# Kernel tuning notes

Hardware: AMD Instinct MI355X
Metric: run time of the kernel (lower is better)

## Reference

```python
import jax, jax.numpy as jnp
import numpy as np

B, S, D, H = 4, 2048, 1024, 16
DH = D // H  # 64
NEG = -1e9


def setup_inputs() -> dict:
    key = jax.random.key(0)
    k1, k2, k3 = jax.random.split(key, 3)
    x = jax.random.normal(k1, (B, S, D), dtype=jnp.float32)
    w_attn = jax.random.normal(k2, (D, 3 * D), dtype=jnp.float32) * 0.02
    b_attn = jnp.zeros((3 * D,), dtype=jnp.float32)
    w_proj = jax.random.normal(k3, (D, D), dtype=jnp.float32) * 0.02
    b_proj = jnp.zeros((D,), dtype=jnp.float32)
    return {"x": x, "w_attn": w_attn, "b_attn": b_attn, "w_proj": w_proj, "b_proj": b_proj}


def reference(x, w_attn, b_attn, w_proj, b_proj):
    # c_attn: fused QKV projection (Conv1D with rf=1 == dense layer)
    qkv = x @ w_attn + b_attn  # [B,S,3D]
    q, k, v = jnp.split(qkv, 3, axis=-1)

    def split_heads(t):  # [B,S,D] -> [B,H,S,DH]
        return t.reshape(B, S, H, DH).transpose(0, 2, 1, 3)

    q, k, v = split_heads(q), split_heads(k), split_heads(v)

    # scaled scores with additive causal mask (as w*b + -1e9*(1-b))
    w = jnp.einsum("bhqd,bhkd->bhqk", q, k) / jnp.sqrt(jnp.float32(DH))
    causal = jnp.tril(jnp.ones((S, S), dtype=w.dtype))[None, None]
    w = w * causal + NEG * (1.0 - causal)
    w = jax.nn.softmax(w, axis=-1)
    # attn_dropout / resid_dropout: p=0 (eval) -> identity

    a = jnp.einsum("bhqk,bhkd->bhqd", w, v)  # [B,H,S,DH]
    a = a.transpose(0, 2, 1, 3).reshape(B, S, D)  # merge heads
    return a @ w_proj + b_proj
```

## Files before the change

### kernel.cpp

```cpp
#include <hip/hip_runtime.h>


typedef short  s8v   __attribute__((ext_vector_type(8)));
typedef float  f32x4 __attribute__((ext_vector_type(4)));
typedef float  f32x16 __attribute__((ext_vector_type(16)));
typedef unsigned short u16;
typedef u16    u16x4 __attribute__((ext_vector_type(4)));
typedef unsigned int u32;
typedef u32    u32x2 __attribute__((ext_vector_type(2)));

__device__ __forceinline__ u16 f2b(float f) {
  union { float f; unsigned u; } v; v.f = f;
  unsigned r = v.u + 0x7FFFu + ((v.u >> 16) & 1u);
  return (u16)(r >> 16);
}
__device__ __forceinline__ u32 cvtpk(float lo, float hi) {
  u32 r; asm("v_cvt_pk_bf16_f32 %0, %1, %2" : "=v"(r) : "v"(lo), "v"(hi)); return r;
}
__device__ __forceinline__ void plswap(u32 &d, u32 &s) {
  asm volatile("v_permlane32_swap_b32 %0, %1" : "+v"(d), "+v"(s));
}
__device__ __forceinline__ void gll16(const void* g, void* l) {
  __builtin_amdgcn_global_load_lds((const __attribute__((address_space(1))) void*)g,
                                   (__attribute__((address_space(3))) void*)l, 16, 0, 0);
}

#define QSCALE 0.18033688011112042f

__global__ __launch_bounds__(256) void k_cvt(const float* __restrict__ in,
                                             u16* __restrict__ out, int n4) {
  int t = blockIdx.x * 256 + threadIdx.x;
  if (t < n4) {
    f32x4 f = ((const f32x4*)in)[t];
    u16x4 o;
    o[0] = f2b(f[0]); o[1] = f2b(f[1]); o[2] = f2b(f[2]); o[3] = f2b(f[3]);
    ((u16x4*)out)[t] = o;
  }
}

__global__ __launch_bounds__(256) void k_tr(const float* __restrict__ in,
                                            u16* __restrict__ out, int R, int C) {
  __shared__ float tile[32][33];
  int c0 = blockIdx.x * 32, r0 = blockIdx.y * 32;
  int tx = threadIdx.x, ty = threadIdx.y;
#pragma unroll
  for (int j = 0; j < 4; j++)
    tile[ty + j * 8][tx] = in[(size_t)(r0 + ty + j * 8) * C + c0 + tx];
  __syncthreads();
#pragma unroll
  for (int j = 0; j < 4; j++)
    out[(size_t)(c0 + ty + j * 8) * R + r0 + tx] = f2b(tile[tx][ty + j * 8]);
}

__device__ __forceinline__ void gemm_tile(const u16* bA, const u16* bB,
                                          f32x4 (&acc)[4][8],
                                          int wr, int wc, int lr, int lg) {
  s8v af[4], bfr[8];
#pragma unroll
  for (int m = 0; m < 4; m++) {
    const int row = wr + m * 16 + lr;
    af[m] = *(const s8v*)&bA[row * 32 + (lg ^ ((row >> 1) & 3)) * 8];
  }
#pragma unroll
  for (int n = 0; n < 8; n++) {
    const int row = wc + n * 16 + lr;
    bfr[n] = *(const s8v*)&bB[row * 32 + (lg ^ ((row >> 1) & 3)) * 8];
  }
  __builtin_amdgcn_s_setprio(1);
#pragma unroll
  for (int m = 0; m < 4; m++)
#pragma unroll
    for (int n = 0; n < 8; n++)
      acc[m][n] = __builtin_amdgcn_mfma_f32_16x16x32_bf16(af[m], bfr[n], acc[m][n], 0, 0, 0);
  __builtin_amdgcn_s_setprio(0);
}

template <int EPI>
__global__ __launch_bounds__(256, 2) void k_gemm(
    const u16* __restrict__ A, const u16* __restrict__ Bt,
    const float* __restrict__ bias,
    u16* __restrict__ qb, u16* __restrict__ kb, u16* __restrict__ vb,
    float* __restrict__ outf, int M, int N, int K) {
  __shared__ u16 lA[3][4096];
  __shared__ u16 lB[3][8192];
  const int tid = threadIdx.x;
  const int lane = tid & 63, w = tid >> 6;
  const int wr = (w >> 1) * 64, wc = (w & 1) * 128;
  const int lr = lane & 15, lg = lane >> 4;

  const int nwg = gridDim.x * gridDim.y;
  const int bid = blockIdx.y * gridDim.x + blockIdx.x;
  const int swz = (bid & 7) * (nwg >> 3) + (bid >> 3);
  const int m0 = (swz / gridDim.x) * 128, n0 = (swz % gridDim.x) * 256;

  const int rr = lane >> 2;
  const int cb = ((lane & 3) ^ ((lane >> 3) & 3)) * 16;
  const size_t K2 = (size_t)K * 2;
  const char* gAc = (const char*)A + (size_t)m0 * K2;
  const char* gBc = (const char*)Bt + (size_t)n0 * K2;

  auto stage = [&](int kt, int buf) {
    const size_t ko = (size_t)kt * 64 + cb;
    char* dA = (char*)&lA[buf][0];
    char* dB = (char*)&lB[buf][0];
#pragma unroll
    for (int i = 0; i < 2; i++) {
      const int sg = 2 * w + i;
      gll16(gAc + (size_t)(16 * sg + rr) * K2 + ko, dA + sg * 1024);
    }
#pragma unroll
    for (int i = 0; i < 4; i++) {
      const int sg = 4 * w + i;
      gll16(gBc + (size_t)(16 * sg + rr) * K2 + ko, dB + sg * 1024);
    }
  };

  f32x4 acc[4][8];
  f32x4 zz = {0.f, 0.f, 0.f, 0.f};
#pragma unroll
  for (int m = 0; m < 4; m++)
#pragma unroll
    for (int n = 0; n < 8; n++) acc[m][n] = zz;

  const int nk = K / 32;
  stage(0, 0);
  if (nk > 1) stage(1, 1);

#define STEP(T, CB, SB)                                                     \
  if ((T) < nk) {                                                           \
    if ((T) + 1 < nk) { asm volatile("s_waitcnt vmcnt(6)" ::: "memory"); }  \
    else              { asm volatile("s_waitcnt vmcnt(0)" ::: "memory"); }  \
    __builtin_amdgcn_s_barrier();                                           \
    __builtin_amdgcn_sched_barrier(0);                                      \
    if ((T) + 2 < nk) stage((T) + 2, (SB));                                 \
    gemm_tile(&lA[(CB)][0], &lB[(CB)][0], acc, wr, wc, lr, lg);             \
  }

  for (int t0 = 0; t0 < nk; t0 += 3) {
    STEP(t0,     0, 2)
    STEP(t0 + 1, 1, 0)
    STEP(t0 + 2, 2, 1)
  }
#undef STEP

#pragma unroll
  for (int m = 0; m < 4; m++) {
#pragma unroll
    for (int n = 0; n < 8; n++) {
      const int col = n0 + wc + n * 16 + lr;
      const float bb = bias[col];
      const int row0 = m0 + wr + m * 16 + 4 * lg;
      if (EPI == 0) {
        const int which = col >> 10, d = col & 1023, h = d >> 6, dh = d & 63;
        if (which == 2) {
          const int b = row0 >> 11, s = row0 & 2047;
          u16x4 ov;
#pragma unroll
          for (int r = 0; r < 4; r++) ov[r] = f2b(acc[m][n][r] + bb);
          *(u16x4*)(vb + ((size_t)((b * 16 + h) * 64 + dh)) * 2048 + s) = ov;
        } else {
          u16* dst = which == 0 ? qb : kb;
          const float sc = which == 0 ? QSCALE : 1.0f;
#pragma unroll
          for (int r = 0; r < 4; r++) {
            const int row = row0 + r;
            const int b = row >> 11, s = row & 2047;
            dst[(size_t)((b * 16 + h) * 2048 + s) * 64 + dh] = f2b((acc[m][n][r] + bb) * sc);
          }
        }
      } else {
#pragma unroll
        for (int r = 0; r < 4; r++)
          outf[(size_t)(row0 + r) * N + col] = acc[m][n][r] + bb;
      }
    }
  }
}

__global__ __launch_bounds__(256, 3) void k_attn(
    const u16* __restrict__ Q, const u16* __restrict__ K,
    const u16* __restrict__ Vt, u16* __restrict__ O) {
  __shared__ u16 lKV[2][8192];
  const int x = blockIdx.x;
  const int bh = ((x & 7) << 3) | ((x >> 3) & 7);
  const int qt = 15 - (x >> 6);
  const int tid = threadIdx.x, lane = tid & 63, w = tid >> 6;
  const int l31 = lane & 31, h = lane >> 5;
  const int qbase = qt * 128 + w * 32;
  const u16* Kb = K + (size_t)bh * 2048 * 64;
  const u16* Vb = Vt + (size_t)bh * 64 * 2048;

  auto stage_dma = [&](int kv0, int buf) {
    char* base = (char*)&lKV[buf][0];
#pragma unroll
    for (int i = 0; i < 2; i++) {
      const int sg = 2 * w + i;
      const int r = lane ^ sg;
      gll16(Kb + (size_t)(kv0 + r) * 64 + sg * 8, base + sg * 1024);
      gll16(Vb + (size_t)r * 2048 + kv0 + sg * 8, base + 8192 + sg * 1024);
    }
  };

  s8v qf[4];
#pragma unroll
  for (int ks = 0; ks < 4; ks++)
    qf[ks] = *(const s8v*)(Q + (size_t)(bh * 2048 + qbase + l31) * 64 + ks * 16 + 8 * h);

  f32x16 accO0, accO1;
#pragma unroll
  for (int i = 0; i < 16; i++) { accO0[i] = 0.f; accO1[i] = 0.f; }
  float mrun = -1e30f, lrun = 0.f;

  const int ntile = 2 * qt + 2;
  stage_dma(0, 0);

  for (int t = 0; t < ntile; ++t) {
    const int kv0 = t * 64;
    asm volatile("s_waitcnt vmcnt(0)" ::: "memory");
    __builtin_amdgcn_s_barrier();
    __builtin_amdgcn_sched_barrier(0);
    if (t + 1 < ntile) stage_dma((t + 1) * 64, (t + 1) & 1);
    const u16* base = &lKV[t & 1][0];

    if (kv0 <= qbase + 31) {
      f32x16 st0, st1;
#pragma unroll
      for (int i = 0; i < 16; i++) { st0[i] = 0.f; st1[i] = 0.f; }
      __builtin_amdgcn_s_setprio(1);
#pragma unroll
      for (int ks = 0; ks < 4; ks++) {
        const int sl = 2 * ks + h;
        s8v a0 = *(const s8v*)&base[(sl * 64 + (l31 ^ sl)) * 8];
        s8v a1 = *(const s8v*)&base[(sl * 64 + ((32 + l31) ^ sl)) * 8];
        st0 = __builtin_amdgcn_mfma_f32_32x32x16_bf16(a0, qf[ks], st0, 0, 0, 0);
        st1 = __builtin_amdgcn_mfma_f32_32x32x16_bf16(a1, qf[ks], st1, 0, 0, 0);
      }
      __builtin_amdgcn_s_setprio(0);
      if (kv0 + 63 > qbase) {
        const int dq = qbase + l31 - kv0;
#pragma unroll
        for (int r = 0; r < 16; r++) {
          const int kl = (r & 3) + 8 * (r >> 2) + 4 * h;
          if (kl > dq) st0[r] = -1e30f;
          if (kl + 32 > dq) st1[r] = -1e30f;
        }
      }
      float mx = st0[0];
#pragma unroll
      for (int r = 1; r < 16; r++) mx = fmaxf(mx, st0[r]);
#pragma unroll
      for (int r = 0; r < 16; r++) mx = fmaxf(mx, st1[r]);
      mx = fmaxf(mx, __shfl_xor(mx, 32));
      if (!__all(mx <= mrun + 11.0f)) {
        const float mnew = fmaxf(mrun, mx);
        const float f = exp2f(mrun - mnew);
        lrun *= f;
#pragma unroll
        for (int r = 0; r < 16; r++) { accO0[r] *= f; accO1[r] *= f; }
        mrun = mnew;
      }
      float s = 0.f;
#pragma unroll
      for (int r = 0; r < 16; r++) { st0[r] = exp2f(st0[r] - mrun); s += st0[r]; }
#pragma unroll
      for (int r = 0; r < 16; r++) { st1[r] = exp2f(st1[r] - mrun); s += st1[r]; }
      s += __shfl_xor(s, 32);
      lrun += s;
      u32 W0[8], W1[8];
#pragma unroll
      for (int a = 0; a < 4; a++) {
        W0[2 * a]     = cvtpk(st0[4 * a], st0[4 * a + 1]);
        W0[2 * a + 1] = cvtpk(st0[4 * a + 2], st0[4 * a + 3]);
        W1[2 * a]     = cvtpk(st1[4 * a], st1[4 * a + 1]);
        W1[2 * a + 1] = cvtpk(st1[4 * a + 2], st1[4 * a + 3]);
      }
      __builtin_amdgcn_s_setprio(1);
#pragma unroll
      for (int ks = 0; ks < 4; ks++) {
        const int kp = ks & 1;
        u32 x0 = (ks < 2) ? W0[4 * kp]     : W1[4 * kp];
        u32 y0 = (ks < 2) ? W0[4 * kp + 2] : W1[4 * kp + 2];
        u32 x1 = (ks < 2) ? W0[4 * kp + 1] : W1[4 * kp + 1];
        u32 y1 = (ks < 2) ? W0[4 * kp + 3] : W1[4 * kp + 3];
        plswap(x0, y0);
        plswap(x1, y1);
        union { u32 u[4]; s8v v; } fb;
        fb.u[0] = x0; fb.u[1] = x1; fb.u[2] = y0; fb.u[3] = y1;
        const int sl = 2 * ks + h;
        s8v va0 = *(const s8v*)&base[4096 + (sl * 64 + (l31 ^ sl)) * 8];
        s8v va1 = *(const s8v*)&base[4096 + (sl * 64 + ((32 + l31) ^ sl)) * 8];
        accO0 = __builtin_amdgcn_mfma_f32_32x32x16_bf16(va0, fb.v, accO0, 0, 0, 0);
        accO1 = __builtin_amdgcn_mfma_f32_32x32x16_bf16(va1, fb.v, accO1, 0, 0, 0);
      }
      __builtin_amdgcn_s_setprio(0);
    }
  }

  const int b_ = bh >> 4, h_ = bh & 15;
  const float rinv = 1.0f / lrun;
  u16* Ob = O + (size_t)(b_ * 2048 + qbase + l31) * 1024 + h_ * 64;
#pragma unroll
  for (int a = 0; a < 4; a++) {
    u32x2 o0, o1;
    o0[0] = cvtpk(accO0[4 * a] * rinv, accO0[4 * a + 1] * rinv);
    o0[1] = cvtpk(accO0[4 * a + 2] * rinv, accO0[4 * a + 3] * rinv);
    o1[0] = cvtpk(accO1[4 * a] * rinv, accO1[4 * a + 1] * rinv);
    o1[1] = cvtpk(accO1[4 * a + 2] * rinv, accO1[4 * a + 3] * rinv);
    *(u32x2*)(Ob + 8 * a + 4 * h) = o0;
    *(u32x2*)(Ob + 32 + 8 * a + 4 * h) = o1;
  }
}

extern "C" void kernel_launch(void* const* d_in, const int* in_sizes, int n_in,
                              void* d_out, int out_size, void* d_ws, size_t ws_size,
                              hipStream_t stream) {
  const float* x      = (const float*)d_in[0];
  const float* w_attn = (const float*)d_in[1];
  const float* b_attn = (const float*)d_in[2];
  const float* w_proj = (const float*)d_in[3];
  const float* b_proj = (const float*)d_in[4];
  float* out = (float*)d_out;

  u16* ws  = (u16*)d_ws;
  u16* xb  = ws;
  u16* wTa = xb + 8388608;
  u16* wTp = wTa + 3145728;
  u16* qb  = wTp + 1048576;
  u16* kb  = qb + 8388608;
  u16* vb  = kb + 8388608;

  k_cvt<<<8192, 256, 0, stream>>>(x, xb, 2097152);
  k_tr<<<dim3(96, 32), dim3(32, 8), 0, stream>>>(w_attn, wTa, 1024, 3072);
  k_tr<<<dim3(32, 32), dim3(32, 8), 0, stream>>>(w_proj, wTp, 1024, 1024);
  k_gemm<0><<<dim3(12, 64), 256, 0, stream>>>(xb, wTa, b_attn, qb, kb, vb, nullptr, 8192, 3072, 1024);
  k_attn<<<1024, 256, 0, stream>>>(qb, kb, vb, xb);
  k_gemm<1><<<dim3(4, 64), 256, 0, stream>>>(xb, wTp, b_proj, nullptr, nullptr, nullptr, out, 8192, 1024, 1024);
}
```

Baseline: 200.7 us.

## Templatize GEMM tiles and use 512-thread blocks with larger QKV tile

Makes the GEMM kernel templated on tile size and occupancy, switching both projections to 8-wave 512-thread workgroups. The QKV projection moves to a 256x256 tile, which raises operand reuse per LDS load and halves the grid. The output projection keeps a 128x256 tile but spreads it over more waves, so each wave holds fewer accumulators. The vmcnt waits are adjusted to the new per-wave load counts. The larger tile raises LDS use and shrinks the grid, which risks lower occupancy or poor tail balance on the 256-CU part.

Measured after the change: 204.8 us. +2.0%, slower.

```diff
diff --git a/kernel.cpp b/kernel.cpp
--- a/kernel.cpp
+++ b/kernel.cpp
@@ -52,46 +52,28 @@
     out[(size_t)(c0 + ty + j * 8) * R + r0 + tx] = f2b(tile[tx][ty + j * 8]);
 }
 
-__device__ __forceinline__ void gemm_tile(const u16* bA, const u16* bB,
-                                          f32x4 (&acc)[4][8],
-                                          int wr, int wc, int lr, int lg) {
-  s8v af[4], bfr[8];
-#pragma unroll
-  for (int m = 0; m < 4; m++) {
-    const int row = wr + m * 16 + lr;
-    af[m] = *(const s8v*)&bA[row * 32 + (lg ^ ((row >> 1) & 3)) * 8];
-  }
-#pragma unroll
-  for (int n = 0; n < 8; n++) {
-    const int row = wc + n * 16 + lr;
-    bfr[n] = *(const s8v*)&bB[row * 32 + (lg ^ ((row >> 1) & 3)) * 8];
-  }
-  __builtin_amdgcn_s_setprio(1);
-#pragma unroll
-  for (int m = 0; m < 4; m++)
-#pragma unroll
-    for (int n = 0; n < 8; n++)
-      acc[m][n] = __builtin_amdgcn_mfma_f32_16x16x32_bf16(af[m], bfr[n], acc[m][n], 0, 0, 0);
-  __builtin_amdgcn_s_setprio(0);
-}
-
-template <int EPI>
-__global__ __launch_bounds__(256, 2) void k_gemm(
+template <int EPI, int BM, int BN, int MINW>
+__global__ __launch_bounds__(512, MINW) void k_gemm(
     const u16* __restrict__ A, const u16* __restrict__ Bt,
     const float* __restrict__ bias,
     u16* __restrict__ qb, u16* __restrict__ kb, u16* __restrict__ vb,
     float* __restrict__ outf, int M, int N, int K) {
-  __shared__ u16 lA[3][4096];
-  __shared__ u16 lB[3][8192];
+  constexpr int MF = BM / 32;
+  constexpr int NF = BN / 64;
+  constexpr int AS = BM / 128;
+  constexpr int BS = BN / 128;
+  constexpr int LPW = AS + BS;
+  __shared__ u16 lA[3][BM * 32];
+  __shared__ u16 lB[3][BN * 32];
   const int tid = threadIdx.x;
   const int lane = tid & 63, w = tid >> 6;
-  const int wr = (w >> 1) * 64, wc = (w & 1) * 128;
+  const int wr = (w >> 2) * (BM / 2), wc = (w & 3) * (BN / 4);
   const int lr = lane & 15, lg = lane >> 4;
 
   const int nwg = gridDim.x * gridDim.y;
   const int bid = blockIdx.y * gridDim.x + blockIdx.x;
   const int swz = (bid & 7) * (nwg >> 3) + (bid >> 3);
-  const int m0 = (swz / gridDim.x) * 128, n0 = (swz % gridDim.x) * 256;
+  const int m0 = (swz / gridDim.x) * BM, n0 = (swz % gridDim.x) * BN;
 
   const int rr = lane >> 2;
   const int cb = ((lane & 3) ^ ((lane >> 3) & 3)) * 16;
@@ -104,36 +86,61 @@
     char* dA = (char*)&lA[buf][0];
     char* dB = (char*)&lB[buf][0];
 #pragma unroll
-    for (int i = 0; i < 2; i++) {
-      const int sg = 2 * w + i;
+    for (int i = 0; i < AS; i++) {
+      const int sg = AS * w + i;
       gll16(gAc + (size_t)(16 * sg + rr) * K2 + ko, dA + sg * 1024);
     }
 #pragma unroll
-    for (int i = 0; i < 4; i++) {
-      const int sg = 4 * w + i;
+    for (int i = 0; i < BS; i++) {
+      const int sg = BS * w + i;
       gll16(gBc + (size_t)(16 * sg + rr) * K2 + ko, dB + sg * 1024);
     }
   };
 
-  f32x4 acc[4][8];
+  auto tile_compute = [&](const u16* bA, const u16* bB, f32x4 (&acc)[MF][NF]) {
+    s8v af[MF], bfr[NF];
+#pragma unroll
+    for (int m = 0; m < MF; m++) {
+      const int row = wr + m * 16 + lr;
+      af[m] = *(const s8v*)&bA[row * 32 + (lg ^ ((row >> 1) & 3)) * 8];
+    }
+#pragma unroll
+    for (int n = 0; n < NF; n++) {
+      const int row = wc + n * 16 + lr;
+      bfr[n] = *(const s8v*)&bB[row * 32 + (lg ^ ((row >> 1) & 3)) * 8];
+    }
+    __builtin_amdgcn_s_setprio(1);
+#pragma unroll
+    for (int m = 0; m < MF; m++)
+#pragma unroll
+      for (int n = 0; n < NF; n++)
+        acc[m][n] = __builtin_amdgcn_mfma_f32_16x16x32_bf16(af[m], bfr[n], acc[m][n], 0, 0, 0);
+    __builtin_amdgcn_s_setprio(0);
+  };
+
+  f32x4 acc[MF][NF];
   f32x4 zz = {0.f, 0.f, 0.f, 0.f};
 #pragma unroll
-  for (int m = 0; m < 4; m++)
-#pragma unroll
-    for (int n = 0; n < 8; n++) acc[m][n] = zz;
+  for (int m = 0; m < MF; m++)
+#pragma unroll
+    for (int n = 0; n < NF; n++) acc[m][n] = zz;
 
   const int nk = K / 32;
   stage(0, 0);
   if (nk > 1) stage(1, 1);
 
-#define STEP(T, CB, SB)                                                     \
-  if ((T) < nk) {                                                           \
-    if ((T) + 1 < nk) { asm volatile("s_waitcnt vmcnt(6)" ::: "memory"); }  \
-    else              { asm volatile("s_waitcnt vmcnt(0)" ::: "memory"); }  \
-    __builtin_amdgcn_s_barrier();                                           \
-    __builtin_amdgcn_sched_barrier(0);                                      \
-    if ((T) + 2 < nk) stage((T) + 2, (SB));                                 \
-    gemm_tile(&lA[(CB)][0], &lB[(CB)][0], acc, wr, wc, lr, lg);             \
+#define STEP(T, CB, SB)                                                      \
+  if ((T) < nk) {                                                            \
+    if ((T) + 1 < nk) {                                                      \
+      if constexpr (LPW == 4) asm volatile("s_waitcnt vmcnt(4)" ::: "memory"); \
+      else                    asm volatile("s_waitcnt vmcnt(3)" ::: "memory"); \
+    } else {                                                                 \
+      asm volatile("s_waitcnt vmcnt(0)" ::: "memory");                       \
+    }                                                                        \
+    __builtin_amdgcn_s_barrier();                                            \
+    __builtin_amdgcn_sched_barrier(0);                                       \
+    if ((T) + 2 < nk) stage((T) + 2, (SB));                                  \
+    tile_compute(&lA[(CB)][0], &lB[(CB)][0], acc);                           \
   }
 
   for (int t0 = 0; t0 < nk; t0 += 3) {
@@ -144,9 +151,9 @@
 #undef STEP
 
 #pragma unroll
-  for (int m = 0; m < 4; m++) {
-#pragma unroll
-    for (int n = 0; n < 8; n++) {
+  for (int m = 0; m < MF; m++) {
+#pragma unroll
+    for (int n = 0; n < NF; n++) {
       const int col = n0 + wc + n * 16 + lr;
       const float bb = bias[col];
       const int row0 = m0 + wr + m * 16 + 4 * lg;
@@ -332,7 +339,9 @@
   k_cvt<<<8192, 256, 0, stream>>>(x, xb, 2097152);
   k_tr<<<dim3(96, 32), dim3(32, 8), 0, stream>>>(w_attn, wTa, 1024, 3072);
   k_tr<<<dim3(32, 32), dim3(32, 8), 0, stream>>>(w_proj, wTp, 1024, 1024);
-  k_gemm<0><<<dim3(12, 64), 256, 0, stream>>>(xb, wTa, b_attn, qb, kb, vb, nullptr, 8192, 3072, 1024);
+  k_gemm<0, 256, 256, 2><<<dim3(12, 32), 512, 0, stream>>>(
+      xb, wTa, b_attn, qb, kb, vb, nullptr, 8192, 3072, 1024);
   k_attn<<<1024, 256, 0, stream>>>(qb, kb, vb, xb);
-  k_gemm<1><<<dim3(4, 64), 256, 0, stream>>>(xb, wTp, b_proj, nullptr, nullptr, nullptr, out, 8192, 1024, 1024);
-}
+  k_gemm<1, 128, 256, 4><<<dim3(4, 64), 512, 0, stream>>>(
+      xb, wTp, b_proj, nullptr, nullptr, nullptr, out, 8192, 1024, 1024);
+}
```

## Restructure GEMM to 256x128 tiles, 8 waves, K=64 stages with split loads

Applied to the files above, without the earlier changes.

Reworks the bf16 GEMM kernel used for the QKV and output projections. The block tile goes from 128x256 to 256x128 and the block grows to 512 threads (8 waves), each computing a 64x64 sub-tile. Each pipeline stage now covers 64 of K, with an 8-way XOR-swizzled LDS layout, and is processed in two phases so the global-to-LDS loads for the stage two ahead are interleaved between the phases. K becomes a template constant so the main loop can be fully unrolled. The aim is better overlap of global loads with MFMA work and less loop overhead, at the cost of more LDS per block (144 KB across three buffers), an extra barrier per phase, and fewer accumulators per wave.

Result: faster. 189.3 us (-5.7%).

```diff
diff --git a/kernel.cpp b/kernel.cpp
--- a/kernel.cpp
+++ b/kernel.cpp
@@ -52,90 +52,91 @@
     out[(size_t)(c0 + ty + j * 8) * R + r0 + tx] = f2b(tile[tx][ty + j * 8]);
 }
 
-__device__ __forceinline__ void gemm_tile(const u16* bA, const u16* bB,
-                                          f32x4 (&acc)[4][8],
-                                          int wr, int wc, int lr, int lg) {
-  s8v af[4], bfr[8];
-#pragma unroll
-  for (int m = 0; m < 4; m++) {
-    const int row = wr + m * 16 + lr;
-    af[m] = *(const s8v*)&bA[row * 32 + (lg ^ ((row >> 1) & 3)) * 8];
-  }
-#pragma unroll
-  for (int n = 0; n < 8; n++) {
-    const int row = wc + n * 16 + lr;
-    bfr[n] = *(const s8v*)&bB[row * 32 + (lg ^ ((row >> 1) & 3)) * 8];
-  }
-  __builtin_amdgcn_s_setprio(1);
-#pragma unroll
-  for (int m = 0; m < 4; m++)
-#pragma unroll
-    for (int n = 0; n < 8; n++)
-      acc[m][n] = __builtin_amdgcn_mfma_f32_16x16x32_bf16(af[m], bfr[n], acc[m][n], 0, 0, 0);
-  __builtin_amdgcn_s_setprio(0);
-}
-
-template <int EPI>
-__global__ __launch_bounds__(256, 2) void k_gemm(
+template <int EPI, int KT>
+__global__ __launch_bounds__(512, 2) void k_gemm(
     const u16* __restrict__ A, const u16* __restrict__ Bt,
     const float* __restrict__ bias,
     u16* __restrict__ qb, u16* __restrict__ kb, u16* __restrict__ vb,
-    float* __restrict__ outf, int M, int N, int K) {
-  __shared__ u16 lA[3][4096];
-  __shared__ u16 lB[3][8192];
+    float* __restrict__ outf, int M, int N) {
+  __shared__ u16 lA[3][256 * 64];
+  __shared__ u16 lB[3][128 * 64];
   const int tid = threadIdx.x;
   const int lane = tid & 63, w = tid >> 6;
-  const int wr = (w >> 1) * 64, wc = (w & 1) * 128;
+  const int wr = (w >> 1) * 64, wc = (w & 1) * 64;
   const int lr = lane & 15, lg = lane >> 4;
 
   const int nwg = gridDim.x * gridDim.y;
   const int bid = blockIdx.y * gridDim.x + blockIdx.x;
   const int swz = (bid & 7) * (nwg >> 3) + (bid >> 3);
-  const int m0 = (swz / gridDim.x) * 128, n0 = (swz % gridDim.x) * 256;
-
-  const int rr = lane >> 2;
-  const int cb = ((lane & 3) ^ ((lane >> 3) & 3)) * 16;
-  const size_t K2 = (size_t)K * 2;
-  const char* gAc = (const char*)A + (size_t)m0 * K2;
-  const char* gBc = (const char*)Bt + (size_t)n0 * K2;
-
-  auto stage = [&](int kt, int buf) {
-    const size_t ko = (size_t)kt * 64 + cb;
-    char* dA = (char*)&lA[buf][0];
-    char* dB = (char*)&lB[buf][0];
-#pragma unroll
-    for (int i = 0; i < 2; i++) {
-      const int sg = 2 * w + i;
-      gll16(gAc + (size_t)(16 * sg + rr) * K2 + ko, dA + sg * 1024);
-    }
-#pragma unroll
-    for (int i = 0; i < 4; i++) {
-      const int sg = 4 * w + i;
-      gll16(gBc + (size_t)(16 * sg + rr) * K2 + ko, dB + sg * 1024);
-    }
+  const int m0 = (swz / gridDim.x) * 256, n0 = (swz % gridDim.x) * 128;
+
+  const size_t K2 = (size_t)KT * 2;
+  const char* gAc = (const char*)A + (size_t)m0 * K2 + (size_t)(lane >> 3) * K2 +
+                    (((lane & 7) ^ (lane >> 3)) * 16);
+  const char* gBc = (const char*)Bt + (size_t)n0 * K2 + (size_t)(lane >> 3) * K2 +
+                    (((lane & 7) ^ (lane >> 3)) * 16);
+
+  auto gllA = [&](int kt, int buf, int i) {
+    const int sg = 4 * w + i;
+    gll16(gAc + (size_t)sg * 8 * K2 + (size_t)kt * 128,
+          (char*)&lA[buf][0] + sg * 1024);
   };
-
-  f32x4 acc[4][8];
+  auto gllB = [&](int kt, int buf, int i) {
+    const int sg = 2 * w + i;
+    gll16(gBc + (size_t)sg * 8 * K2 + (size_t)kt * 128,
+          (char*)&lB[buf][0] + sg * 1024);
+  };
+
+  f32x4 acc[4][4];
   f32x4 zz = {0.f, 0.f, 0.f, 0.f};
 #pragma unroll
   for (int m = 0; m < 4; m++)
 #pragma unroll
-    for (int n = 0; n < 8; n++) acc[m][n] = zz;
-
-  const int nk = K / 32;
-  stage(0, 0);
-  if (nk > 1) stage(1, 1);
-
-#define STEP(T, CB, SB)                                                     \
-  if ((T) < nk) {                                                           \
-    if ((T) + 1 < nk) { asm volatile("s_waitcnt vmcnt(6)" ::: "memory"); }  \
-    else              { asm volatile("s_waitcnt vmcnt(0)" ::: "memory"); }  \
-    __builtin_amdgcn_s_barrier();                                           \
-    __builtin_amdgcn_sched_barrier(0);                                      \
-    if ((T) + 2 < nk) stage((T) + 2, (SB));                                 \
-    gemm_tile(&lA[(CB)][0], &lB[(CB)][0], acc, wr, wc, lr, lg);             \
-  }
-
+    for (int n = 0; n < 4; n++) acc[m][n] = zz;
+
+  auto phase = [&](const u16* bA, const u16* bB, int ks) {
+    s8v af[4], bf[4];
+#pragma unroll
+    for (int n = 0; n < 4; n++) {
+      const int row = wc + n * 16 + lr;
+      bf[n] = *(const s8v*)&bB[row * 64 + (((ks << 2) | lg) ^ (row & 7)) * 8];
+    }
+#pragma unroll
+    for (int m = 0; m < 4; m++) {
+      const int row = wr + m * 16 + lr;
+      af[m] = *(const s8v*)&bA[row * 64 + (((ks << 2) | lg) ^ (row & 7)) * 8];
+    }
+    asm volatile("s_waitcnt lgkmcnt(0)" ::: "memory");
+    __builtin_amdgcn_sched_barrier(0);
+    __builtin_amdgcn_s_setprio(1);
+#pragma unroll
+    for (int m = 0; m < 4; m++)
+#pragma unroll
+      for (int n = 0; n < 4; n++)
+        acc[m][n] = __builtin_amdgcn_mfma_f32_16x16x32_bf16(af[m], bf[n], acc[m][n], 0, 0, 0);
+    __builtin_amdgcn_s_setprio(0);
+    __builtin_amdgcn_s_barrier();
+  };
+
+  constexpr int nk = KT / 64;
+  gllA(0, 0, 0); gllA(0, 0, 1); gllA(0, 0, 2); gllA(0, 0, 3);
+  gllB(0, 0, 0); gllB(0, 0, 1);
+  gllA(1, 1, 0); gllA(1, 1, 1); gllA(1, 1, 2); gllA(1, 1, 3);
+  gllB(1, 1, 0); gllB(1, 1, 1);
+
+#define STEP(T, CB, SB)                                                        \
+  if ((T) < nk) {                                                              \
+    if ((T) + 1 < nk) asm volatile("s_waitcnt vmcnt(6)" ::: "memory");         \
+    else              asm volatile("s_waitcnt vmcnt(0)" ::: "memory");         \
+    __builtin_amdgcn_s_barrier();                                              \
+    __builtin_amdgcn_sched_barrier(0);                                         \
+    if ((T) + 2 < nk) { gllA((T)+2,(SB),0); gllA((T)+2,(SB),1); gllB((T)+2,(SB),0); } \
+    phase(&lA[(CB)][0], &lB[(CB)][0], 0);                                      \
+    if ((T) + 2 < nk) { gllA((T)+2,(SB),2); gllA((T)+2,(SB),3); gllB((T)+2,(SB),1); } \
+    phase(&lA[(CB)][0], &lB[(CB)][0], 1);                                      \
+  }
+
+#pragma unroll
   for (int t0 = 0; t0 < nk; t0 += 3) {
     STEP(t0,     0, 2)
     STEP(t0 + 1, 1, 0)
@@ -146,7 +147,7 @@
 #pragma unroll
   for (int m = 0; m < 4; m++) {
 #pragma unroll
-    for (int n = 0; n < 8; n++) {
+    for (int n = 0; n < 4; n++) {
       const int col = n0 + wc + n * 16 + lr;
       const float bb = bias[col];
       const int row0 = m0 + wr + m * 16 + 4 * lg;
@@ -332,7 +333,9 @@
   k_cvt<<<8192, 256, 0, stream>>>(x, xb, 2097152);
   k_tr<<<dim3(96, 32), dim3(32, 8), 0, stream>>>(w_attn, wTa, 1024, 3072);
   k_tr<<<dim3(32, 32), dim3(32, 8), 0, stream>>>(w_proj, wTp, 1024, 1024);
-  k_gemm<0><<<dim3(12, 64), 256, 0, stream>>>(xb, wTa, b_attn, qb, kb, vb, nullptr, 8192, 3072, 1024);
+  k_gemm<0, 1024><<<dim3(24, 32), 512, 0, stream>>>(
+      xb, wTa, b_attn, qb, kb, vb, nullptr, 8192, 3072);
   k_attn<<<1024, 256, 0, stream>>>(qb, kb, vb, xb);
-  k_gemm<1><<<dim3(4, 64), 256, 0, stream>>>(xb, wTp, b_proj, nullptr, nullptr, nullptr, out, 8192, 1024, 1024);
-}
+  k_gemm<1, 1024><<<dim3(8, 32), 512, 0, stream>>>(
+      xb, wTp, b_proj, nullptr, nullptr, nullptr, out, 8192, 1024);
+}
```

## Use 256x256 eight-wave pipelined GEMM for QKV and smaller tiles for projection

Applied to the files above, without the earlier changes.

Adds a new 512-thread QKV GEMM kernel with 256x256 tiles, a 64-wide K step held in a double-buffered LDS layout, and a fine-grained schedule that interleaves global-to-LDS loads, LDS reads and MFMA halves under barriers. The aim is to raise data reuse per tile and overlap memory traffic with matrix math. The output projection GEMM is retuned to 128x128 tiles at three blocks per CU, giving more workgroups on the narrow N=1024 problem. The trade-offs are one workgroup per CU for the QKV kernel, a heavy barrier count, and a hardcoded K loop (16 steps of 64, so K must be 1024).

Result: faster. 184.1 us (-8.3%).

```diff
diff --git a/kernel.cpp b/kernel.cpp
--- a/kernel.cpp
+++ b/kernel.cpp
@@ -52,17 +52,166 @@
     out[(size_t)(c0 + ty + j * 8) * R + r0 + tx] = f2b(tile[tx][ty + j * 8]);
 }
 
+template <int KDIM>
+__global__ __launch_bounds__(512, 1) void k_gemm8(
+    const u16* __restrict__ A, const u16* __restrict__ Bt,
+    const float* __restrict__ bias,
+    u16* __restrict__ qb, u16* __restrict__ kb, u16* __restrict__ vb) {
+  __shared__ u16 L[2][4][8192];
+  const int tid = threadIdx.x;
+  const int lane = tid & 63, w = tid >> 6;
+  const int wm = w >> 2, wn = w & 3;
+  const int lr = lane & 15, lg = lane >> 4;
+  const int rIn = lane >> 3;
+  const int cSwz = ((lane & 7) ^ (lane >> 3)) * 16;
+
+  const int nwg = gridDim.x * gridDim.y;
+  const int bid = blockIdx.y * gridDim.x + blockIdx.x;
+  const int swz = (bid & 7) * (nwg >> 3) + (bid >> 3);
+  const int m0 = (swz / gridDim.x) * 256, n0 = (swz % gridDim.x) * 256;
+
+  const size_t K2 = (size_t)KDIM * 2;
+  const char* gAc = (const char*)A + (size_t)m0 * K2;
+  const char* gBc = (const char*)Bt + (size_t)n0 * K2;
+
+#define STAGE2(KT, BUF, SLOT) do {                                             \
+    const char* g_ = ((SLOT) < 2 ? gAc : gBc);                                 \
+    const int h_ = (SLOT) & 1;                                                 \
+    _Pragma("unroll") for (int i_ = 0; i_ < 2; i_++) {                         \
+      const int sg_ = 8 * i_ + w;                                              \
+      gll16(g_ + (size_t)(h_ * 128 + 8 * sg_ + rIn) * K2 +                     \
+                (size_t)(KT) * 128 + cSwz,                                     \
+            (char*)&L[BUF][SLOT][0] + sg_ * 1024);                             \
+    }                                                                          \
+  } while (0)
+
+  s8v af[8], bf[4];
+#define READS(BUF, KS) do {                                                    \
+    const u16* As_ = &L[BUF][wm][0];                                           \
+    const u16* Bs_ = &L[BUF][2 + (wn >> 1)][0];                                \
+    _Pragma("unroll") for (int m_ = 0; m_ < 8; m_++) {                         \
+      const int r_ = m_ * 16 + lr;                                             \
+      af[m_] = *(const s8v*)&As_[r_ * 64 + ((((KS) << 2) | lg) ^ (r_ & 7)) * 8]; } \
+    _Pragma("unroll") for (int n_ = 0; n_ < 4; n_++) {                         \
+      const int r_ = (wn & 1) * 64 + n_ * 16 + lr;                             \
+      bf[n_] = *(const s8v*)&Bs_[r_ * 64 + ((((KS) << 2) | lg) ^ (r_ & 7)) * 8]; } \
+  } while (0)
+
+  f32x4 acc[8][4];
+#pragma unroll
+  for (int m = 0; m < 8; m++)
+#pragma unroll
+    for (int n = 0; n < 4; n++) acc[m][n] = (f32x4){0.f, 0.f, 0.f, 0.f};
+
+#define MFMAH(MH)                                                              \
+  __builtin_amdgcn_s_setprio(1);                                               \
+  _Pragma("unroll") for (int mm_ = 0; mm_ < 4; mm_++)                          \
+  _Pragma("unroll") for (int nn_ = 0; nn_ < 4; nn_++)                          \
+    acc[(MH) * 4 + mm_][nn_] = __builtin_amdgcn_mfma_f32_16x16x32_bf16(        \
+        af[(MH) * 4 + mm_], bf[nn_], acc[(MH) * 4 + mm_][nn_], 0, 0, 0);       \
+  __builtin_amdgcn_s_setprio(0);
+
+  STAGE2(0, 0, 0); STAGE2(0, 0, 1); STAGE2(0, 0, 2); STAGE2(0, 0, 3);
+  asm volatile("s_waitcnt vmcnt(0)" ::: "memory");
+  __builtin_amdgcn_s_barrier();
+
+  for (int j = 0; j < 8; ++j) {
+    const int tO = 2 * j + 1, tE = 2 * j + 2;
+    STAGE2(tO, 1, 0);
+    asm volatile("s_waitcnt vmcnt(2)" ::: "memory");
+    __builtin_amdgcn_s_barrier();
+    __builtin_amdgcn_sched_barrier(0);
+    READS(0, 0);
+    asm volatile("s_waitcnt lgkmcnt(0)" ::: "memory");
+    __builtin_amdgcn_sched_barrier(0);
+    MFMAH(0)
+    __builtin_amdgcn_s_barrier();
+    STAGE2(tO, 1, 1);
+    __builtin_amdgcn_s_barrier();
+    MFMAH(1)
+    __builtin_amdgcn_s_barrier();
+    STAGE2(tO, 1, 2);
+    READS(0, 1);
+    asm volatile("s_waitcnt lgkmcnt(8)" ::: "memory");
+    __builtin_amdgcn_s_barrier();
+    asm volatile("s_waitcnt lgkmcnt(0)" ::: "memory");
+    __builtin_amdgcn_sched_barrier(0);
+    MFMAH(0)
+    __builtin_amdgcn_s_barrier();
+    STAGE2(tO, 1, 3);
+    __builtin_amdgcn_s_barrier();
+    MFMAH(1)
+    __builtin_amdgcn_s_barrier();
+    if (j < 7) {
+      STAGE2(tE, 0, 0);
+      asm volatile("s_waitcnt vmcnt(2)" ::: "memory");
+    } else {
+      asm volatile("s_waitcnt vmcnt(0)" ::: "memory");
+    }
+    __builtin_amdgcn_s_barrier();
+    __builtin_amdgcn_sched_barrier(0);
+    READS(1, 0);
+    asm volatile("s_waitcnt lgkmcnt(0)" ::: "memory");
+    __builtin_amdgcn_sched_barrier(0);
+    MFMAH(0)
+    __builtin_amdgcn_s_barrier();
+    if (j < 7) STAGE2(tE, 0, 1);
+    __builtin_amdgcn_s_barrier();
+    MFMAH(1)
+    __builtin_amdgcn_s_barrier();
+    if (j < 7) STAGE2(tE, 0, 2);
+    READS(1, 1);
+    asm volatile("s_waitcnt lgkmcnt(8)" ::: "memory");
+    __builtin_amdgcn_s_barrier();
+    asm volatile("s_waitcnt lgkmcnt(0)" ::: "memory");
+    __builtin_amdgcn_sched_barrier(0);
+    MFMAH(0)
+    __builtin_amdgcn_s_barrier();
+    if (j < 7) STAGE2(tE, 0, 3);
+    __builtin_amdgcn_s_barrier();
+    MFMAH(1)
+    __builtin_amdgcn_s_barrier();
+  }
+#undef STAGE2
+#undef READS
+#undef MFMAH
+
+#pragma unroll
+  for (int m = 0; m < 8; m++) {
+#pragma unroll
+    for (int n = 0; n < 4; n++) {
+      const int col = n0 + wn * 64 + n * 16 + lr;
+      const float bb = bias[col];
+      const int row0 = m0 + wm * 128 + m * 16 + 4 * lg;
+      const int which = col >> 10, d = col & 1023, hh = d >> 6, dh = d & 63;
+      const int b = row0 >> 11, s = row0 & 2047;
+      if (which == 2) {
+        u16x4 ov;
+#pragma unroll
+        for (int r = 0; r < 4; r++) ov[r] = f2b(acc[m][n][r] + bb);
+        *(u16x4*)(vb + ((size_t)((b * 16 + hh) * 64 + dh)) * 2048 + s) = ov;
+      } else {
+        u16* dst = which == 0 ? qb : kb;
+        const float sc = which == 0 ? QSCALE : 1.0f;
+#pragma unroll
+        for (int r = 0; r < 4; r++)
+          dst[(size_t)((b * 16 + hh) * 2048 + s + r) * 64 + dh] = f2b((acc[m][n][r] + bb) * sc);
+      }
+    }
+  }
+}
+
 __device__ __forceinline__ void gemm_tile(const u16* bA, const u16* bB,
-                                          f32x4 (&acc)[4][8],
+                                          f32x4 (&acc)[4][4],
                                           int wr, int wc, int lr, int lg) {
-  s8v af[4], bfr[8];
+  s8v af[4], bfr[4];
 #pragma unroll
   for (int m = 0; m < 4; m++) {
     const int row = wr + m * 16 + lr;
     af[m] = *(const s8v*)&bA[row * 32 + (lg ^ ((row >> 1) & 3)) * 8];
   }
 #pragma unroll
-  for (int n = 0; n < 8; n++) {
+  for (int n = 0; n < 4; n++) {
     const int row = wc + n * 16 + lr;
     bfr[n] = *(const s8v*)&bB[row * 32 + (lg ^ ((row >> 1) & 3)) * 8];
   }
@@ -70,28 +219,25 @@
 #pragma unroll
   for (int m = 0; m < 4; m++)
 #pragma unroll
-    for (int n = 0; n < 8; n++)
+    for (int n = 0; n < 4; n++)
       acc[m][n] = __builtin_amdgcn_mfma_f32_16x16x32_bf16(af[m], bfr[n], acc[m][n], 0, 0, 0);
   __builtin_amdgcn_s_setprio(0);
 }
 
-template <int EPI>
-__global__ __launch_bounds__(256, 2) void k_gemm(
+__global__ __launch_bounds__(256, 3) void k_gemmP(
     const u16* __restrict__ A, const u16* __restrict__ Bt,
-    const float* __restrict__ bias,
-    u16* __restrict__ qb, u16* __restrict__ kb, u16* __restrict__ vb,
-    float* __restrict__ outf, int M, int N, int K) {
+    const float* __restrict__ bias, float* __restrict__ outf, int M, int N, int K) {
   __shared__ u16 lA[3][4096];
-  __shared__ u16 lB[3][8192];
+  __shared__ u16 lB[3][4096];
   const int tid = threadIdx.x;
   const int lane = tid & 63, w = tid >> 6;
-  const int wr = (w >> 1) * 64, wc = (w & 1) * 128;
+  const int wr = (w >> 1) * 64, wc = (w & 1) * 64;
   const int lr = lane & 15, lg = lane >> 4;
 
   const int nwg = gridDim.x * gridDim.y;
   const int bid = blockIdx.y * gridDim.x + blockIdx.x;
   const int swz = (bid & 7) * (nwg >> 3) + (bid >> 3);
-  const int m0 = (swz / gridDim.x) * 128, n0 = (swz % gridDim.x) * 256;
+  const int m0 = (swz / gridDim.x) * 128, n0 = (swz % gridDim.x) * 128;
 
   const int rr = lane >> 2;
   const int cb = ((lane & 3) ^ ((lane >> 3) & 3)) * 16;
@@ -103,24 +249,17 @@
     const size_t ko = (size_t)kt * 64 + cb;
     char* dA = (char*)&lA[buf][0];
     char* dB = (char*)&lB[buf][0];
-#pragma unroll
-    for (int i = 0; i < 2; i++) {
-      const int sg = 2 * w + i;
-      gll16(gAc + (size_t)(16 * sg + rr) * K2 + ko, dA + sg * 1024);
-    }
-#pragma unroll
-    for (int i = 0; i < 4; i++) {
-      const int sg = 4 * w + i;
-      gll16(gBc + (size_t)(16 * sg + rr) * K2 + ko, dB + sg * 1024);
-    }
+    gll16(gAc + (size_t)(32 * w + rr) * K2 + ko,      dA + (2 * w) * 1024);
+    gll16(gAc + (size_t)(32 * w + 16 + rr) * K2 + ko, dA + (2 * w + 1) * 1024);
+    gll16(gBc + (size_t)(32 * w + rr) * K2 + ko,      dB + (2 * w) * 1024);
+    gll16(gBc + (size_t)(32 * w + 16 + rr) * K2 + ko, dB + (2 * w + 1) * 1024);
   };
 
-  f32x4 acc[4][8];
-  f32x4 zz = {0.f, 0.f, 0.f, 0.f};
+  f32x4 acc[4][4];
 #pragma unroll
   for (int m = 0; m < 4; m++)
 #pragma unroll
-    for (int n = 0; n < 8; n++) acc[m][n] = zz;
+    for (int n = 0; n < 4; n++) acc[m][n] = (f32x4){0.f, 0.f, 0.f, 0.f};
 
   const int nk = K / 32;
   stage(0, 0);
@@ -128,7 +267,7 @@
 
 #define STEP(T, CB, SB)                                                     \
   if ((T) < nk) {                                                           \
-    if ((T) + 1 < nk) { asm volatile("s_waitcnt vmcnt(6)" ::: "memory"); }  \
+    if ((T) + 1 < nk) { asm volatile("s_waitcnt vmcnt(4)" ::: "memory"); }  \
     else              { asm volatile("s_waitcnt vmcnt(0)" ::: "memory"); }  \
     __builtin_amdgcn_s_barrier();                                           \
     __builtin_amdgcn_sched_barrier(0);                                      \
@@ -146,33 +285,13 @@
 #pragma unroll
   for (int m = 0; m < 4; m++) {
 #pragma unroll
-    for (int n = 0; n < 8; n++) {
+    for (int n = 0; n < 4; n++) {
       const int col = n0 + wc + n * 16 + lr;
       const float bb = bias[col];
       const int row0 = m0 + wr + m * 16 + 4 * lg;
-      if (EPI == 0) {
-        const int which = col >> 10, d = col & 1023, h = d >> 6, dh = d & 63;
-        if (which == 2) {
-          const int b = row0 >> 11, s = row0 & 2047;
-          u16x4 ov;
-#pragma unroll
-          for (int r = 0; r < 4; r++) ov[r] = f2b(acc[m][n][r] + bb);
-          *(u16x4*)(vb + ((size_t)((b * 16 + h) * 64 + dh)) * 2048 + s) = ov;
-        } else {
-          u16* dst = which == 0 ? qb : kb;
-          const float sc = which == 0 ? QSCALE : 1.0f;
-#pragma unroll
-          for (int r = 0; r < 4; r++) {
-            const int row = row0 + r;
-            const int b = row >> 11, s = row & 2047;
-            dst[(size_t)((b * 16 + h) * 2048 + s) * 64 + dh] = f2b((acc[m][n][r] + bb) * sc);
-          }
-        }
-      } else {
-#pragma unroll
-        for (int r = 0; r < 4; r++)
-          outf[(size_t)(row0 + r) * N + col] = acc[m][n][r] + bb;
-      }
+#pragma unroll
+      for (int r = 0; r < 4; r++)
+        outf[(size_t)(row0 + r) * N + col] = acc[m][n][r] + bb;
     }
   }
 }
@@ -332,7 +451,7 @@
   k_cvt<<<8192, 256, 0, stream>>>(x, xb, 2097152);
   k_tr<<<dim3(96, 32), dim3(32, 8), 0, stream>>>(w_attn, wTa, 1024, 3072);
   k_tr<<<dim3(32, 32), dim3(32, 8), 0, stream>>>(w_proj, wTp, 1024, 1024);
-  k_gemm<0><<<dim3(12, 64), 256, 0, stream>>>(xb, wTa, b_attn, qb, kb, vb, nullptr, 8192, 3072, 1024);
+  k_gemm8<1024><<<dim3(12, 32), 512, 0, stream>>>(xb, wTa, b_attn, qb, kb, vb);
   k_attn<<<1024, 256, 0, stream>>>(qb, kb, vb, xb);
-  k_gemm<1><<<dim3(4, 64), 256, 0, stream>>>(xb, wTp, b_proj, nullptr, nullptr, nullptr, out, 8192, 1024, 1024);
-}
+  k_gemmP<<<dim3(8, 64), 256, 0, stream>>>(xb, wTp, b_proj, out, 8192, 1024, 1024);
+}
```
